# Kernel tuning notes

Hardware: AMD Instinct MI355X
Metric: run time of the kernel (lower is better)

## Reference

```python
import jax, jax.numpy as jnp
import numpy as np

B, NV, NK = 256, 10475, 144
MV, MK = 778, 21
NB, KN = 8192, 9
TOT_ITR, SW = 5, 0.5


def axis_angle_to_matrix(aa):
    # Rodrigues formula, aa: [B,3] -> [B,3,3]
    angle = jnp.linalg.norm(aa, axis=-1, keepdims=True)
    axis = aa / (angle + 1e-8)
    x, y, z = axis[..., 0], axis[..., 1], axis[..., 2]
    c = jnp.cos(angle[..., 0]); s = jnp.sin(angle[..., 0]); C = 1.0 - c
    R = jnp.stack([
        jnp.stack([c + x * x * C, x * y * C - z * s, x * z * C + y * s], -1),
        jnp.stack([y * x * C + z * s, c + y * y * C, y * z * C - x * s], -1),
        jnp.stack([z * x * C - y * s, z * y * C + x * s, c + z * z * C], -1)], -2)
    return R


def rigid_align(X, Y):
    # Umeyama w/o scale (pytorch3d corresponding_points_alignment): X @ R + T ~= Y
    muX = X.mean(1, keepdims=True); muY = Y.mean(1, keepdims=True)
    C = jnp.einsum('bni,bnj->bij', X - muX, Y - muY)
    U, S, Vt = jnp.linalg.svd(C)
    d = jnp.sign(jnp.linalg.det(U) * jnp.linalg.det(Vt))
    e = jnp.stack([jnp.ones_like(d), jnp.ones_like(d), d], -1)
    R = jnp.einsum('bij,bj,bjk->bik', U, e, Vt)
    T = muY[:, 0] - jnp.einsum('bi,bij->bj', muX[:, 0], R)
    return R, T


def combine_smplx_mano(smplx_vert, smplx_kpt, rv, rk, rpose, lv, lk, lpose,
                       rigid_align_idx, r_align_smplx, l_align_smplx,
                       rhand_vertex_idx, lhand_vertex_idx, r_kpt_idx, l_kpt_idx):
    # undo hand root rotation (torch.inverse on rotation matrices)
    Rr = jnp.linalg.inv(axis_angle_to_matrix(rpose))
    rv = jnp.einsum('bij,bnj->bni', Rr, rv); rk = jnp.einsum('bij,bnj->bni', Rr, rk)
    Rl = jnp.linalg.inv(axis_angle_to_matrix(lpose))
    lv = jnp.einsum('bij,bnj->bni', Rl, lv); lk = jnp.einsum('bij,bnj->bni', Rl, lk)
    # rigid alignment of MANO keypoints to SMPL-X hand keypoints
    R, T = rigid_align(rk[:, rigid_align_idx], smplx_kpt[:, r_align_smplx])
    rv = jnp.einsum('bni,bij->bnj', rv, R) + T[:, None]
    rk = jnp.einsum('bni,bij->bnj', rk, R) + T[:, None]
    R, T = rigid_align(lk[:, rigid_align_idx], smplx_kpt[:, l_align_smplx])
    lv = jnp.einsum('bni,bij->bnj', lv, R) + T[:, None]
    lk = jnp.einsum('bni,bij->bnj', lk, R) + T[:, None]
    # scatter MANO verts/kpts into SMPL-X mesh (torch scatter_ -> .at[].set)
    smplx_vert = smplx_vert.at[:, rhand_vertex_idx].set(rv)
    smplx_vert = smplx_vert.at[:, lhand_vertex_idx].set(lv)
    smplx_kpt = smplx_kpt.at[:, r_kpt_idx].set(rk)
    smplx_kpt = smplx_kpt.at[:, l_kpt_idx].set(lk)
    return smplx_vert, smplx_kpt


def smooth_hand_boundary(v, hand_boundary_idx, vert_neighbor_idxs):
    vn = vert_neighbor_idxs[hand_boundary_idx]                     # [NB, KN]
    mask = vn != -1
    safe = jnp.where(mask, vn, 0)
    num_valid = jnp.maximum(mask.sum(-1), 1).astype(v.dtype)        # [NB]
    maskf = mask.astype(v.dtype)[None, :, :, None]
    for _ in range(TOT_ITR):
        npos = v[:, safe] * maskf                                   # [B, NB, KN, 3]
        nmean = npos.sum(2) / num_valid[None, :, None]
        upd = (1.0 - SW) * v[:, hand_boundary_idx] + SW * nmean
        v = v.at[:, hand_boundary_idx].set(upd)
    return v


def setup_inputs():
    key = jax.random.key(0)
    k = jax.random.split(key, 8)
    rng = np.random.default_rng(0)
    vperm = rng.permutation(NV)
    kperm = rng.permutation(NK)
    vn = rng.integers(0, NV, size=(NV, KN))
    vn[rng.random((NV, KN)) < 0.2] = -1  # -1 padding like smpl_x.vert_neighbor_idxs
    return {
        'smplx_vert_cam': jax.random.normal(k[0], (B, NV, 3), jnp.float32),
        'smplx_kpt_cam': jax.random.normal(k[1], (B, NK, 3), jnp.float32),
        'rmano_vert_cam': jax.random.normal(k[2], (B, MV, 3), jnp.float32),
        'rmano_kpt_cam': jax.random.normal(k[3], (B, MK, 3), jnp.float32),
        'rhand_root_pose': jax.random.normal(k[4], (B, 3), jnp.float32),
        'lmano_vert_cam': jax.random.normal(k[5], (B, MV, 3), jnp.float32),
        'lmano_kpt_cam': jax.random.normal(k[6], (B, MK, 3), jnp.float32),
        'lhand_root_pose': jax.random.normal(k[7], (B, 3), jnp.float32),
        'rigid_align_idx': jnp.asarray(rng.permutation(MK), jnp.int32),
        'r_align_smplx': jnp.asarray(kperm[:MK], jnp.int32),
        'l_align_smplx': jnp.asarray(kperm[MK:2 * MK], jnp.int32),
        'rhand_vertex_idx': jnp.asarray(vperm[:MV], jnp.int32),
        'lhand_vertex_idx': jnp.asarray(vperm[MV:2 * MV], jnp.int32),
        'r_kpt_idx': jnp.asarray(kperm[:MK], jnp.int32),
        'l_kpt_idx': jnp.asarray(kperm[MK:2 * MK], jnp.int32),
        'hand_boundary_idx': jnp.asarray(rng.choice(NV, NB, replace=False), jnp.int32),
        'vert_neighbor_idxs': jnp.asarray(vn, jnp.int32),
    }


def reference(smplx_vert_cam, smplx_kpt_cam, rmano_vert_cam, rmano_kpt_cam,
              rhand_root_pose, lmano_vert_cam, lmano_kpt_cam, lhand_root_pose,
              rigid_align_idx, r_align_smplx, l_align_smplx,
              rhand_vertex_idx, lhand_vertex_idx, r_kpt_idx, l_kpt_idx,
              hand_boundary_idx, vert_neighbor_idxs):
    v, _ = combine_smplx_mano(
        smplx_vert_cam, smplx_kpt_cam, rmano_vert_cam, rmano_kpt_cam,
        rhand_root_pose, lmano_vert_cam, lmano_kpt_cam, lhand_root_pose,
        rigid_align_idx, r_align_smplx, l_align_smplx,
        rhand_vertex_idx, lhand_vertex_idx, r_kpt_idx, l_kpt_idx)
    v = smooth_hand_boundary(v, hand_boundary_idx, vert_neighbor_idxs)
    return v
```

## Files before the change

### kernel.cpp

```cpp
#include <hip/hip_runtime.h>

#define BB    256
#define NVERT 10475
#define NKPT  144
#define MVERT 778
#define MKPT  21
#define NBDRY 8192
#define KNB   9
#define ITERS 5
#define NV3   (NVERT * 3)
#define MV3   (MVERT * 3)

typedef float f32x4 __attribute__((ext_vector_type(4)));

static __device__ __forceinline__ float bfu(unsigned hi16) {
    return __uint_as_float(hi16);
}
static __device__ __forceinline__ unsigned f2bf(float f) {
    unsigned u = __float_as_uint(f);
    u += 0x7FFFu + ((u >> 16) & 1u);
    return u >> 16;
}

static __device__ __forceinline__ void pack_one(unsigned short* msh16, unsigned p, float val) {
    unsigned v = p / 3u;
    unsigned c = p - v * 3u;
    msh16[v * 4u + c] = (unsigned short)f2bf(val);
}

static __device__ __forceinline__ void stage_load(const float* __restrict__ g,
                                                  float* sh, int n, int t, int nt) {
    unsigned lead = (4u - ((unsigned)(((size_t)g) >> 2) & 3u)) & 3u;
    unsigned nb4 = ((unsigned)n - lead) >> 2;
    if (t == 0) for (unsigned e = 0; e < lead; ++e) sh[e] = g[e];
    if (t == 1) for (unsigned e = lead + 4u * nb4; e < (unsigned)n; ++e) sh[e] = g[e];
    const f32x4* g4 = (const f32x4*)(g + lead);
    for (unsigned i4 = (unsigned)t; i4 < nb4; i4 += (unsigned)nt) {
        f32x4 q = g4[i4];
        unsigned p = lead + 4u * i4;
        sh[p] = q.x; sh[p + 1] = q.y; sh[p + 2] = q.z; sh[p + 3] = q.w;
    }
}

static __device__ void compute_align(
    int b, int h,
    const float* __restrict__ skpt, const float* __restrict__ rkpt,
    const float* __restrict__ lkpt, const float* __restrict__ rpose,
    const float* __restrict__ lpose, const int* __restrict__ perm,
    const int* __restrict__ ralign, const int* __restrict__ lalign,
    float* o)
{
    const float* pose = (h ? lpose : rpose) + b * 3;
    const float* kpt  = (h ? lkpt : rkpt) + (size_t)b * MKPT * 3;
    const int* alidx  = h ? lalign : ralign;

    float ax = pose[0], ay = pose[1], az = pose[2];
    float ang = sqrtf(ax*ax + ay*ay + az*az);
    float ia = 1.0f / (ang + 1e-8f);
    float x = ax*ia, y = ay*ia, z = az*ia;
    float c = cosf(ang), s = sinf(ang), Cc = 1.0f - c;
    float A00 = c + x*x*Cc,   A01 = x*y*Cc - z*s, A02 = x*z*Cc + y*s;
    float A10 = y*x*Cc + z*s, A11 = c + y*y*Cc,   A12 = y*z*Cc - x*s;
    float A20 = z*x*Cc - y*s, A21 = z*y*Cc + x*s, A22 = c + z*z*Cc;

    float sX0=0,sX1=0,sX2=0, sY0=0,sY1=0,sY2=0;
    float S00=0,S01=0,S02=0,S10=0,S11=0,S12=0,S20=0,S21=0,S22=0;
    for (int n = 0; n < MKPT; ++n) {
        int pi = perm[n];
        float p0 = kpt[pi*3+0], p1 = kpt[pi*3+1], p2 = kpt[pi*3+2];
        float X0 = A00*p0 + A10*p1 + A20*p2;
        float X1 = A01*p0 + A11*p1 + A21*p2;
        float X2 = A02*p0 + A12*p1 + A22*p2;
        int qi = alidx[n];
        const float* yp = skpt + ((size_t)b * NKPT + qi) * 3;
        float Y0 = yp[0], Y1 = yp[1], Y2 = yp[2];
        sX0 += X0; sX1 += X1; sX2 += X2;
        sY0 += Y0; sY1 += Y1; sY2 += Y2;
        S00 += X0*Y0; S01 += X0*Y1; S02 += X0*Y2;
        S10 += X1*Y0; S11 += X1*Y1; S12 += X1*Y2;
        S20 += X2*Y0; S21 += X2*Y1; S22 += X2*Y2;
    }
    const float invN = 1.0f / (float)MKPT;
    float C00 = S00 - sX0*sY0*invN, C01 = S01 - sX0*sY1*invN, C02 = S02 - sX0*sY2*invN;
    float C10 = S10 - sX1*sY0*invN, C11 = S11 - sX1*sY1*invN, C12 = S12 - sX1*sY2*invN;
    float C20 = S20 - sX2*sY0*invN, C21 = S21 - sX2*sY1*invN, C22 = S22 - sX2*sY2*invN;

    float N[4][4];
    N[0][0] = C00 + C11 + C22;
    N[0][1] = C21 - C12; N[0][2] = C02 - C20; N[0][3] = C10 - C01;
    N[1][1] = C00 - C11 - C22; N[1][2] = C01 + C10; N[1][3] = C02 + C20;
    N[2][2] = -C00 + C11 - C22; N[2][3] = C12 + C21;
    N[3][3] = -C00 - C11 + C22;
    N[1][0] = N[0][1]; N[2][0] = N[0][2]; N[3][0] = N[0][3];
    N[2][1] = N[1][2]; N[3][1] = N[1][3]; N[3][2] = N[2][3];

    float V[4][4] = {{1,0,0,0},{0,1,0,0},{0,0,1,0},{0,0,0,1}};
    for (int sweep = 0; sweep < 10; ++sweep) {
        float off = N[0][1]*N[0][1] + N[0][2]*N[0][2] + N[0][3]*N[0][3]
                  + N[1][2]*N[1][2] + N[1][3]*N[1][3] + N[2][3]*N[2][3];
        if (off < 1e-12f) break;
        #pragma unroll
        for (int p = 0; p < 3; ++p) {
            #pragma unroll
            for (int q = p + 1; q < 4; ++q) {
                float apq = N[p][q];
                if (fabsf(apq) > 1e-30f) {
                    float theta = (N[q][q] - N[p][p]) / (2.0f * apq);
                    float tt = copysignf(1.0f, theta) / (fabsf(theta) + sqrtf(theta*theta + 1.0f));
                    float cj = rsqrtf(tt*tt + 1.0f);
                    float sj = tt * cj;
                    #pragma unroll
                    for (int k = 0; k < 4; ++k) {
                        float akp = N[k][p], akq = N[k][q];
                        N[k][p] = cj*akp - sj*akq;
                        N[k][q] = sj*akp + cj*akq;
                    }
                    #pragma unroll
                    for (int k = 0; k < 4; ++k) {
                        float apk = N[p][k], aqk = N[q][k];
                        N[p][k] = cj*apk - sj*aqk;
                        N[q][k] = sj*apk + cj*aqk;
                    }
                    #pragma unroll
                    for (int k = 0; k < 4; ++k) {
                        float vkp = V[k][p], vkq = V[k][q];
                        V[k][p] = cj*vkp - sj*vkq;
                        V[k][q] = sj*vkp + cj*vkq;
                    }
                }
            }
        }
    }
    int m = 0;
    float lmax = N[0][0];
    if (N[1][1] > lmax) { lmax = N[1][1]; m = 1; }
    if (N[2][2] > lmax) { lmax = N[2][2]; m = 2; }
    if (N[3][3] > lmax) { lmax = N[3][3]; m = 3; }
    float w = V[0][m], qx = V[1][m], qy = V[2][m], qz = V[3][m];

    float R00 = 1.0f - 2.0f*(qy*qy + qz*qz), R01 = 2.0f*(qx*qy - w*qz), R02 = 2.0f*(qx*qz + w*qy);
    float R10 = 2.0f*(qx*qy + w*qz), R11 = 1.0f - 2.0f*(qx*qx + qz*qz), R12 = 2.0f*(qy*qz - w*qx);
    float R20 = 2.0f*(qx*qz - w*qy), R21 = 2.0f*(qy*qz + w*qx), R22 = 1.0f - 2.0f*(qx*qx + qy*qy);

    float mX0 = sX0*invN, mX1 = sX1*invN, mX2 = sX2*invN;
    float mY0 = sY0*invN, mY1 = sY1*invN, mY2 = sY2*invN;

    o[0]  = A00*R00 + A01*R10 + A02*R20;
    o[1]  = A00*R01 + A01*R11 + A02*R21;
    o[2]  = A00*R02 + A01*R12 + A02*R22;
    o[3]  = A10*R00 + A11*R10 + A12*R20;
    o[4]  = A10*R01 + A11*R11 + A12*R21;
    o[5]  = A10*R02 + A11*R12 + A12*R22;
    o[6]  = A20*R00 + A21*R10 + A22*R20;
    o[7]  = A20*R01 + A21*R11 + A22*R21;
    o[8]  = A20*R02 + A21*R12 + A22*R22;
    o[9]  = mY0 - (mX0*R00 + mX1*R10 + mX2*R20);
    o[10] = mY1 - (mX0*R01 + mX1*R11 + mX2*R21);
    o[11] = mY2 - (mX0*R02 + mX1*R12 + mX2*R22);
}

__global__ __launch_bounds__(1024, 1) void fused_kernel(
    const float* __restrict__ svert,
    const float* __restrict__ skpt,
    const float* __restrict__ rv,
    const float* __restrict__ rkpt,
    const float* __restrict__ rpose,
    const float* __restrict__ lv,
    const float* __restrict__ lkpt,
    const float* __restrict__ lpose,
    const int*   __restrict__ perm,
    const int*   __restrict__ ralign,
    const int*   __restrict__ lalign,
    const int*   __restrict__ ridx,
    const int*   __restrict__ lidx,
    const int*   __restrict__ bidx,
    const int*   __restrict__ vnbr,
    float*       __restrict__ out)
{
    __shared__ __align__(16) unsigned short msh16[(NVERT + 1) * 4];
    __shared__ __align__(16) float hstage[2 * MV3];
    __shared__ float affsh[24];
    const int b = blockIdx.x;
    const int tid = threadIdx.x;

    if (tid < 2) {
        compute_align(b, tid, skpt, rkpt, lkpt, rpose, lpose,
                      perm, ralign, lalign, affsh + tid * 12);
    } else if (tid == 2) {
        *((uint2*)(msh16 + NVERT * 4)) = make_uint2(0u, 0u);
    } else if (tid >= 64) {
        const int t = tid - 64;
        const float* g = svert + (size_t)b * NV3;
        unsigned lead = (4u - ((unsigned)(((size_t)g) >> 2) & 3u)) & 3u;
        unsigned nb4 = ((unsigned)NV3 - lead) >> 2;
        if (t == 0) for (unsigned e = 0; e < lead; ++e) pack_one(msh16, e, g[e]);
        if (t == 1) for (unsigned e = lead + 4u * nb4; e < (unsigned)NV3; ++e) pack_one(msh16, e, g[e]);
        const f32x4* g4 = (const f32x4*)(g + lead);
        for (unsigned i4 = (unsigned)t; i4 < nb4; i4 += 960u) {
            f32x4 q = g4[i4];
            unsigned p = lead + 4u * i4;
            pack_one(msh16, p,     q.x);
            pack_one(msh16, p + 1, q.y);
            pack_one(msh16, p + 2, q.z);
            pack_one(msh16, p + 3, q.w);
        }
        stage_load(rv + (size_t)b * MV3, hstage,       MV3, t, 960);
        stage_load(lv + (size_t)b * MV3, hstage + MV3, MV3, t, 960);
    }

    unsigned w0[8], w1[8], w2[8], w3[8], w4[8];
    #pragma unroll
    for (int k = 0; k < 8; ++k) {
        int j = k * 1024 + tid;
        int bi = bidx[j];
        const int* row = vnbr + (size_t)bi * KNB;
        unsigned n[9]; unsigned cnt = 0;
        #pragma unroll
        for (int e = 0; e < 9; ++e) {
            int vv = row[e];
            if (vv >= 0) { n[e] = (unsigned)vv; ++cnt; }
            else         { n[e] = (unsigned)NVERT; }
        }
        if (cnt == 0) cnt = 1;
        w0[k] = n[0] | (n[1] << 14);
        w1[k] = n[2] | (n[3] << 14);
        w2[k] = n[4] | (n[5] << 14);
        w3[k] = n[6] | (n[7] << 14);
        w4[k] = n[8] | ((unsigned)bi << 14) | (cnt << 28);
    }
    __syncthreads();

    for (int i = tid; i < 2 * MVERT; i += 1024) {
        int h = (i >= MVERT) ? 1 : 0;
        int nn = i - h * MVERT;
        const int* hidx = h ? lidx : ridx;
        const float* M = affsh + h * 12;
        const float* p = hstage + h * MV3 + nn * 3;
        float p0 = p[0], p1 = p[1], p2 = p[2];
        float o0 = p0 * M[0] + p1 * M[3] + p2 * M[6] + M[9];
        float o1 = p0 * M[1] + p1 * M[4] + p2 * M[7] + M[10];
        float o2 = p0 * M[2] + p1 * M[5] + p2 * M[8] + M[11];
        ((uint2*)msh16)[hidx[nn]] = make_uint2(f2bf(o0) | (f2bf(o1) << 16), f2bf(o2));
    }
    __syncthreads();

    const uint2* mesh = (const uint2*)msh16;

#define NB_GATHER(idx) { uint2 m = mesh[(idx)]; \
        sx += bfu(m.x << 16); sy += bfu(m.x & 0xFFFF0000u); sz += bfu(m.y << 16); }
    for (int itr = 0; itr < ITERS; ++itr) {
        uint2 up[8];
        #pragma unroll
        for (int k = 0; k < 8; ++k) {
            float sx = 0.f, sy = 0.f, sz = 0.f;
            NB_GATHER(w0[k] & 0x3FFFu);
            NB_GATHER((w0[k] >> 14) & 0x3FFFu);
            NB_GATHER(w1[k] & 0x3FFFu);
            NB_GATHER((w1[k] >> 14) & 0x3FFFu);
            NB_GATHER(w2[k] & 0x3FFFu);
            NB_GATHER((w2[k] >> 14) & 0x3FFFu);
            NB_GATHER(w3[k] & 0x3FFFu);
            NB_GATHER((w3[k] >> 14) & 0x3FFFu);
            NB_GATHER(w4[k] & 0x3FFFu);
            uint2 ms = mesh[(w4[k] >> 14) & 0x3FFFu];
            float hinv = 0.5f * __builtin_amdgcn_rcpf((float)(w4[k] >> 28));
            float ux = 0.5f * bfu(ms.x << 16)         + hinv * sx;
            float uy = 0.5f * bfu(ms.x & 0xFFFF0000u) + hinv * sy;
            float uz = 0.5f * bfu(ms.y << 16)         + hinv * sz;
            up[k] = make_uint2(f2bf(ux) | (f2bf(uy) << 16), f2bf(uz));
        }
        __syncthreads();
        #pragma unroll
        for (int k = 0; k < 8; ++k) {
            ((uint2*)msh16)[(w4[k] >> 14) & 0x3FFFu] = up[k];
        }
        __syncthreads();
    }
#undef NB_GATHER

    float* dst = out + (size_t)b * NV3;
    const unsigned lead = (4u - ((unsigned)(((size_t)dst) >> 2) & 3u)) & 3u;
#define COMP(i, val) { unsigned v_ = (i) / 3u; unsigned c_ = (i) - v_ * 3u; \
        uint2 m_ = mesh[v_]; \
        val = (c_ == 0u) ? bfu(m_.x << 16) : (c_ == 1u) ? bfu(m_.x & 0xFFFF0000u) : bfu(m_.y << 16); }
    if ((unsigned)tid < lead) {
        float v; COMP((unsigned)tid, v);
        dst[tid] = v;
    }
    const unsigned nb4 = ((unsigned)NV3 - lead) >> 2;
    f32x4* dst4 = (f32x4*)(dst + lead);
    for (unsigned i4 = (unsigned)tid; i4 < nb4; i4 += 1024u) {
        unsigned i0 = lead + 4u * i4;
        f32x4 o;
        COMP(i0 + 0u, o.x);
        COMP(i0 + 1u, o.y);
        COMP(i0 + 2u, o.z);
        COMP(i0 + 3u, o.w);
        dst4[i4] = o;
    }
    const unsigned done = lead + 4u * nb4;
    if ((unsigned)tid < (unsigned)NV3 - done) {
        float v; COMP(done + (unsigned)tid, v);
        dst[done + tid] = v;
    }
#undef COMP
}

extern "C" void kernel_launch(void* const* d_in, const int* in_sizes, int n_in,
                              void* d_out, int out_size, void* d_ws, size_t ws_size,
                              hipStream_t stream) {
    const float* svert  = (const float*)d_in[0];
    const float* skpt   = (const float*)d_in[1];
    const float* rv     = (const float*)d_in[2];
    const float* rk     = (const float*)d_in[3];
    const float* rpose  = (const float*)d_in[4];
    const float* lv     = (const float*)d_in[5];
    const float* lk     = (const float*)d_in[6];
    const float* lpose  = (const float*)d_in[7];
    const int*   perm   = (const int*)d_in[8];
    const int*   ralign = (const int*)d_in[9];
    const int*   lalign = (const int*)d_in[10];
    const int*   ridx   = (const int*)d_in[11];
    const int*   lidx   = (const int*)d_in[12];
    const int*   bidx   = (const int*)d_in[15];
    const int*   vnbr   = (const int*)d_in[16];
    float* out = (float*)d_out;

    fused_kernel<<<BB, 1024, 0, stream>>>(svert, skpt, rv, rk, rpose,
                                          lv, lk, lpose, perm, ralign, lalign,
                                          ridx, lidx, bidx, vnbr, out);
}
```

Before: 68.83 us.

## Precompute alignment and neighbor tables in a setup kernel before the fused smoothing kernel

Adds a small setup kernel that computes the per-batch rigid-alignment affines and the packed boundary-neighbor index table once, writing both to workspace. Previously every block redid the neighbor packing and ran the serial SVD alignment on two threads. The main kernel now reads these precomputed values, so all 1024 threads take part in the mesh load. It also keeps each boundary vertex's own value in registers across iterations, removing one LDS read per update, which is valid because only that thread writes the vertex. The cost is an extra kernel launch and the global round trip of the table.

After: 64.17 us. -6.8%, faster.

```diff
diff --git a/kernel.cpp b/kernel.cpp
--- a/kernel.cpp
+++ b/kernel.cpp
@@ -159,22 +159,47 @@
     o[11] = mY2 - (mX0*R02 + mX1*R12 + mX2*R22);
 }
 
+__global__ __launch_bounds__(128) void setup_kernel(
+    const float* __restrict__ skpt, const float* __restrict__ rkpt,
+    const float* __restrict__ lkpt, const float* __restrict__ rpose,
+    const float* __restrict__ lpose, const int* __restrict__ perm,
+    const int* __restrict__ ralign, const int* __restrict__ lalign,
+    const int* __restrict__ bidx, const int* __restrict__ vnbr,
+    float* __restrict__ aff, unsigned* __restrict__ tab)
+{
+    const int g = blockIdx.x;
+    if (g < 4) {
+        int t = g * 128 + threadIdx.x;
+        compute_align(t >> 1, t & 1, skpt, rkpt, lkpt, rpose, lpose,
+                      perm, ralign, lalign, aff + t * 12);
+        return;
+    }
+    int j = (g - 4) * 128 + threadIdx.x;
+    int bi = bidx[j];
+    const int* row = vnbr + (size_t)bi * KNB;
+    unsigned n[9]; unsigned cnt = 0;
+    #pragma unroll
+    for (int e = 0; e < 9; ++e) {
+        int vv = row[e];
+        if (vv >= 0) { n[e] = (unsigned)vv; ++cnt; }
+        else         { n[e] = (unsigned)NVERT; }
+    }
+    if (cnt == 0) cnt = 1;
+    tab[0 * NBDRY + j] = n[0] | (n[1] << 14);
+    tab[1 * NBDRY + j] = n[2] | (n[3] << 14);
+    tab[2 * NBDRY + j] = n[4] | (n[5] << 14);
+    tab[3 * NBDRY + j] = n[6] | (n[7] << 14);
+    tab[4 * NBDRY + j] = n[8] | ((unsigned)bi << 14) | (cnt << 28);
+}
+
 __global__ __launch_bounds__(1024, 1) void fused_kernel(
     const float* __restrict__ svert,
-    const float* __restrict__ skpt,
     const float* __restrict__ rv,
-    const float* __restrict__ rkpt,
-    const float* __restrict__ rpose,
     const float* __restrict__ lv,
-    const float* __restrict__ lkpt,
-    const float* __restrict__ lpose,
-    const int*   __restrict__ perm,
-    const int*   __restrict__ ralign,
-    const int*   __restrict__ lalign,
     const int*   __restrict__ ridx,
     const int*   __restrict__ lidx,
-    const int*   __restrict__ bidx,
-    const int*   __restrict__ vnbr,
+    const float* __restrict__ aff,
+    const unsigned* __restrict__ tab,
     float*       __restrict__ out)
 {
     __shared__ __align__(16) unsigned short msh16[(NVERT + 1) * 4];
@@ -183,20 +208,16 @@
     const int b = blockIdx.x;
     const int tid = threadIdx.x;
 
-    if (tid < 2) {
-        compute_align(b, tid, skpt, rkpt, lkpt, rpose, lpose,
-                      perm, ralign, lalign, affsh + tid * 12);
-    } else if (tid == 2) {
-        *((uint2*)(msh16 + NVERT * 4)) = make_uint2(0u, 0u);
-    } else if (tid >= 64) {
-        const int t = tid - 64;
+    if (tid == 0) *((uint2*)(msh16 + NVERT * 4)) = make_uint2(0u, 0u);
+    if (tid < 24) affsh[tid] = aff[b * 24 + tid];
+    {
         const float* g = svert + (size_t)b * NV3;
         unsigned lead = (4u - ((unsigned)(((size_t)g) >> 2) & 3u)) & 3u;
         unsigned nb4 = ((unsigned)NV3 - lead) >> 2;
-        if (t == 0) for (unsigned e = 0; e < lead; ++e) pack_one(msh16, e, g[e]);
-        if (t == 1) for (unsigned e = lead + 4u * nb4; e < (unsigned)NV3; ++e) pack_one(msh16, e, g[e]);
+        if (tid == 0) for (unsigned e = 0; e < lead; ++e) pack_one(msh16, e, g[e]);
+        if (tid == 1) for (unsigned e = lead + 4u * nb4; e < (unsigned)NV3; ++e) pack_one(msh16, e, g[e]);
         const f32x4* g4 = (const f32x4*)(g + lead);
-        for (unsigned i4 = (unsigned)t; i4 < nb4; i4 += 960u) {
+        for (unsigned i4 = (unsigned)tid; i4 < nb4; i4 += 1024u) {
             f32x4 q = g4[i4];
             unsigned p = lead + 4u * i4;
             pack_one(msh16, p,     q.x);
@@ -204,29 +225,18 @@
             pack_one(msh16, p + 2, q.z);
             pack_one(msh16, p + 3, q.w);
         }
-        stage_load(rv + (size_t)b * MV3, hstage,       MV3, t, 960);
-        stage_load(lv + (size_t)b * MV3, hstage + MV3, MV3, t, 960);
-    }
-
+        stage_load(rv + (size_t)b * MV3, hstage,       MV3, tid, 1024);
+        stage_load(lv + (size_t)b * MV3, hstage + MV3, MV3, tid, 1024);
+    }
     unsigned w0[8], w1[8], w2[8], w3[8], w4[8];
     #pragma unroll
     for (int k = 0; k < 8; ++k) {
         int j = k * 1024 + tid;
-        int bi = bidx[j];
-        const int* row = vnbr + (size_t)bi * KNB;
-        unsigned n[9]; unsigned cnt = 0;
-        #pragma unroll
-        for (int e = 0; e < 9; ++e) {
-            int vv = row[e];
-            if (vv >= 0) { n[e] = (unsigned)vv; ++cnt; }
-            else         { n[e] = (unsigned)NVERT; }
-        }
-        if (cnt == 0) cnt = 1;
-        w0[k] = n[0] | (n[1] << 14);
-        w1[k] = n[2] | (n[3] << 14);
-        w2[k] = n[4] | (n[5] << 14);
-        w3[k] = n[6] | (n[7] << 14);
-        w4[k] = n[8] | ((unsigned)bi << 14) | (cnt << 28);
+        w0[k] = tab[j];
+        w1[k] = tab[NBDRY + j];
+        w2[k] = tab[2 * NBDRY + j];
+        w3[k] = tab[3 * NBDRY + j];
+        w4[k] = tab[4 * NBDRY + j];
     }
     __syncthreads();
 
@@ -246,10 +256,13 @@
 
     const uint2* mesh = (const uint2*)msh16;
 
+    uint2 up[8];
+    #pragma unroll
+    for (int k = 0; k < 8; ++k) up[k] = mesh[(w4[k] >> 14) & 0x3FFFu];
+
 #define NB_GATHER(idx) { uint2 m = mesh[(idx)]; \
         sx += bfu(m.x << 16); sy += bfu(m.x & 0xFFFF0000u); sz += bfu(m.y << 16); }
     for (int itr = 0; itr < ITERS; ++itr) {
-        uint2 up[8];
         #pragma unroll
         for (int k = 0; k < 8; ++k) {
             float sx = 0.f, sy = 0.f, sz = 0.f;
@@ -262,11 +275,10 @@
             NB_GATHER(w3[k] & 0x3FFFu);
             NB_GATHER((w3[k] >> 14) & 0x3FFFu);
             NB_GATHER(w4[k] & 0x3FFFu);
-            uint2 ms = mesh[(w4[k] >> 14) & 0x3FFFu];
             float hinv = 0.5f * __builtin_amdgcn_rcpf((float)(w4[k] >> 28));
-            float ux = 0.5f * bfu(ms.x << 16)         + hinv * sx;
-            float uy = 0.5f * bfu(ms.x & 0xFFFF0000u) + hinv * sy;
-            float uz = 0.5f * bfu(ms.y << 16)         + hinv * sz;
+            float ux = 0.5f * bfu(up[k].x << 16)         + hinv * sx;
+            float uy = 0.5f * bfu(up[k].x & 0xFFFF0000u) + hinv * sy;
+            float uz = 0.5f * bfu(up[k].y << 16)         + hinv * sz;
             up[k] = make_uint2(f2bf(ux) | (f2bf(uy) << 16), f2bf(uz));
         }
         __syncthreads();
@@ -326,7 +338,12 @@
     const int*   vnbr   = (const int*)d_in[16];
     float* out = (float*)d_out;
 
-    fused_kernel<<<BB, 1024, 0, stream>>>(svert, skpt, rv, rk, rpose,
-                                          lv, lk, lpose, perm, ralign, lalign,
-                                          ridx, lidx, bidx, vnbr, out);
-}
+    float*    aff = (float*)d_ws;
+    unsigned* tab = (unsigned*)((char*)d_ws + 24576);
+
+    setup_kernel<<<68, 128, 0, stream>>>(skpt, rk, lk, rpose, lpose,
+                                         perm, ralign, lalign, bidx, vnbr,
+                                         aff, tab);
+    fused_kernel<<<BB, 1024, 0, stream>>>(svert, rv, lv, ridx, lidx,
+                                          aff, tab, out);
+}
```

## Precompute static neighbor sums once and gather only dynamic boundary neighbors per iteration

Applied to the files above, without the earlier changes.

A new pre-kernel builds a per-boundary-vertex table that splits neighbors into those that belong to the boundary set (and change across iterations) and those that do not (and stay constant). The main kernel sums the static neighbors once into shared memory and re-gathers only the dynamic neighbors in each of the five smoothing iterations, cutting LDS gather traffic. It also vectorizes the bf16 mesh pack and unpack so that whole 12-float groups are handled per thread. The cost is an extra kernel launch, a larger shared-memory pool, and one more bf16 rounding on the static partial sum, which could shift numerics slightly.

Result: slower. 84.96 us (+23.4%).

```diff
diff --git a/kernel.cpp b/kernel.cpp
--- a/kernel.cpp
+++ b/kernel.cpp
@@ -21,7 +21,9 @@
     u += 0x7FFFu + ((u >> 16) & 1u);
     return u >> 16;
 }
-
+static __device__ __forceinline__ uint2 packv(float x, float y, float z) {
+    return make_uint2(f2bf(x) | (f2bf(y) << 16), f2bf(z));
+}
 static __device__ __forceinline__ void pack_one(unsigned short* msh16, unsigned p, float val) {
     unsigned v = p / 3u;
     unsigned c = p - v * 3u;
@@ -159,6 +161,40 @@
     o[11] = mY2 - (mX0*R02 + mX1*R12 + mX2*R22);
 }
 
+__global__ __launch_bounds__(128) void pack_kernel(
+    const int* __restrict__ bidx, const int* __restrict__ vnbr,
+    unsigned* __restrict__ tab)
+{
+    __shared__ unsigned char flag[NVERT];
+    const int tid = threadIdx.x;
+    for (int i = tid; i < NVERT; i += 128) flag[i] = 0;
+    __syncthreads();
+    for (int j = tid; j < NBDRY; j += 128) flag[bidx[j]] = 1;
+    __syncthreads();
+    int j = blockIdx.x * 128 + tid;
+    int bi = bidx[j];
+    const int* row = vnbr + (size_t)bi * KNB;
+    unsigned slot[9];
+    #pragma unroll
+    for (int e = 0; e < 9; ++e) slot[e] = (unsigned)NVERT;
+    int dc = 0, sc = 0;
+    #pragma unroll
+    for (int e = 0; e < 9; ++e) {
+        int v = row[e];
+        if (v >= 0) {
+            if (flag[v]) slot[dc++] = (unsigned)v;
+            else         slot[8 - (sc++)] = (unsigned)v;
+        }
+    }
+    unsigned vcnt = (unsigned)(dc + sc);
+    if (vcnt == 0u) vcnt = 1u;
+    tab[0 * NBDRY + j] = slot[0] | (slot[1] << 14) | ((unsigned)dc << 28);
+    tab[1 * NBDRY + j] = slot[2] | (slot[3] << 14) | (vcnt << 28);
+    tab[2 * NBDRY + j] = slot[4] | (slot[5] << 14);
+    tab[3 * NBDRY + j] = slot[6] | (slot[7] << 14);
+    tab[4 * NBDRY + j] = slot[8] | ((unsigned)bi << 14) | ((unsigned)sc << 28);
+}
+
 __global__ __launch_bounds__(1024, 1) void fused_kernel(
     const float* __restrict__ svert,
     const float* __restrict__ skpt,
@@ -173,13 +209,15 @@
     const int*   __restrict__ lalign,
     const int*   __restrict__ ridx,
     const int*   __restrict__ lidx,
-    const int*   __restrict__ bidx,
-    const int*   __restrict__ vnbr,
+    const unsigned* __restrict__ tab,
     float*       __restrict__ out)
 {
-    __shared__ __align__(16) unsigned short msh16[(NVERT + 1) * 4];
-    __shared__ __align__(16) float hstage[2 * MV3];
+    __shared__ __align__(16) unsigned long long pool64[(83808 + 65536) / 8];
     __shared__ float affsh[24];
+    unsigned short* msh16 = (unsigned short*)pool64;
+    uint2* meshw = (uint2*)pool64;
+    float* hstage = (float*)((char*)pool64 + 83808);
+    uint2* ssum   = (uint2*)((char*)pool64 + 83808);
     const int b = blockIdx.x;
     const int tid = threadIdx.x;
 
@@ -187,22 +225,47 @@
         compute_align(b, tid, skpt, rkpt, lkpt, rpose, lpose,
                       perm, ralign, lalign, affsh + tid * 12);
     } else if (tid == 2) {
-        *((uint2*)(msh16 + NVERT * 4)) = make_uint2(0u, 0u);
+        meshw[NVERT] = make_uint2(0u, 0u);
     } else if (tid >= 64) {
         const int t = tid - 64;
         const float* g = svert + (size_t)b * NV3;
         unsigned lead = (4u - ((unsigned)(((size_t)g) >> 2) & 3u)) & 3u;
-        unsigned nb4 = ((unsigned)NV3 - lead) >> 2;
-        if (t == 0) for (unsigned e = 0; e < lead; ++e) pack_one(msh16, e, g[e]);
-        if (t == 1) for (unsigned e = lead + 4u * nb4; e < (unsigned)NV3; ++e) pack_one(msh16, e, g[e]);
-        const f32x4* g4 = (const f32x4*)(g + lead);
-        for (unsigned i4 = (unsigned)t; i4 < nb4; i4 += 960u) {
-            f32x4 q = g4[i4];
-            unsigned p = lead + 4u * i4;
-            pack_one(msh16, p,     q.x);
-            pack_one(msh16, p + 1, q.y);
-            pack_one(msh16, p + 2, q.z);
-            pack_one(msh16, p + 3, q.w);
+        unsigned r0 = lead % 3u;
+        unsigned qb = (lead - r0) / 3u;
+        unsigned ng = ((unsigned)NV3 - lead) / 12u;
+        const f32x4* s4 = (const f32x4*)(g + lead);
+        if (t == 0) for (unsigned d = 0; d < lead; ++d) pack_one(msh16, d, g[d]);
+        if (t == 1) for (unsigned d = lead + 12u * ng; d < (unsigned)NV3; ++d) pack_one(msh16, d, g[d]);
+        if (r0 == 0u) {
+            for (unsigned gi = (unsigned)t; gi < ng; gi += 960u) {
+                f32x4 a = s4[3*gi], c = s4[3*gi+1], e = s4[3*gi+2];
+                unsigned q = qb + 4u * gi;
+                meshw[q]     = packv(a.x, a.y, a.z);
+                meshw[q + 1] = packv(a.w, c.x, c.y);
+                meshw[q + 2] = packv(c.z, c.w, e.x);
+                meshw[q + 3] = packv(e.y, e.z, e.w);
+            }
+        } else if (r0 == 1u) {
+            for (unsigned gi = (unsigned)t; gi < ng; gi += 960u) {
+                f32x4 a = s4[3*gi], c = s4[3*gi+1], e = s4[3*gi+2];
+                unsigned q = qb + 4u * gi;
+                msh16[4u*q + 1] = (unsigned short)f2bf(a.x);
+                msh16[4u*q + 2] = (unsigned short)f2bf(a.y);
+                meshw[q + 1] = packv(a.z, a.w, c.x);
+                meshw[q + 2] = packv(c.y, c.z, c.w);
+                meshw[q + 3] = packv(e.x, e.y, e.z);
+                msh16[4u*(q + 4)] = (unsigned short)f2bf(e.w);
+            }
+        } else {
+            for (unsigned gi = (unsigned)t; gi < ng; gi += 960u) {
+                f32x4 a = s4[3*gi], c = s4[3*gi+1], e = s4[3*gi+2];
+                unsigned q = qb + 4u * gi;
+                msh16[4u*q + 2] = (unsigned short)f2bf(a.x);
+                meshw[q + 1] = packv(a.y, a.z, a.w);
+                meshw[q + 2] = packv(c.x, c.y, c.z);
+                meshw[q + 3] = packv(c.w, e.x, e.y);
+                ((unsigned*)msh16)[2u*(q + 4)] = f2bf(e.z) | (f2bf(e.w) << 16);
+            }
         }
         stage_load(rv + (size_t)b * MV3, hstage,       MV3, t, 960);
         stage_load(lv + (size_t)b * MV3, hstage + MV3, MV3, t, 960);
@@ -212,21 +275,11 @@
     #pragma unroll
     for (int k = 0; k < 8; ++k) {
         int j = k * 1024 + tid;
-        int bi = bidx[j];
-        const int* row = vnbr + (size_t)bi * KNB;
-        unsigned n[9]; unsigned cnt = 0;
-        #pragma unroll
-        for (int e = 0; e < 9; ++e) {
-            int vv = row[e];
-            if (vv >= 0) { n[e] = (unsigned)vv; ++cnt; }
-            else         { n[e] = (unsigned)NVERT; }
-        }
-        if (cnt == 0) cnt = 1;
-        w0[k] = n[0] | (n[1] << 14);
-        w1[k] = n[2] | (n[3] << 14);
-        w2[k] = n[4] | (n[5] << 14);
-        w3[k] = n[6] | (n[7] << 14);
-        w4[k] = n[8] | ((unsigned)bi << 14) | (cnt << 28);
+        w0[k] = tab[j];
+        w1[k] = tab[NBDRY + j];
+        w2[k] = tab[2 * NBDRY + j];
+        w3[k] = tab[3 * NBDRY + j];
+        w4[k] = tab[4 * NBDRY + j];
     }
     __syncthreads();
 
@@ -240,70 +293,106 @@
         float o0 = p0 * M[0] + p1 * M[3] + p2 * M[6] + M[9];
         float o1 = p0 * M[1] + p1 * M[4] + p2 * M[7] + M[10];
         float o2 = p0 * M[2] + p1 * M[5] + p2 * M[8] + M[11];
-        ((uint2*)msh16)[hidx[nn]] = make_uint2(f2bf(o0) | (f2bf(o1) << 16), f2bf(o2));
+        meshw[hidx[nn]] = packv(o0, o1, o2);
     }
     __syncthreads();
 
-    const uint2* mesh = (const uint2*)msh16;
-
-#define NB_GATHER(idx) { uint2 m = mesh[(idx)]; \
-        sx += bfu(m.x << 16); sy += bfu(m.x & 0xFFFF0000u); sz += bfu(m.y << 16); }
+#define ADD3(IDX, X, Y, Z) { uint2 m_ = meshw[(IDX)]; \
+        X += bfu(m_.x << 16); Y += bfu(m_.x & 0xFFFF0000u); Z += bfu(m_.y << 16); }
+
+    uint2 up[8];
+    #pragma unroll
+    for (int k = 0; k < 8; ++k) {
+        unsigned a0 = w0[k], a1 = w1[k], a2 = w2[k], a3 = w3[k], a4 = w4[k];
+        up[k] = meshw[(a4 >> 14) & 0x3FFFu];
+        int sc = (int)(a4 >> 28);
+        float tx = 0.f, ty = 0.f, tz = 0.f;
+        if (sc > 0) ADD3(a4 & 0x3FFFu, tx, ty, tz)
+        if (sc > 1) ADD3((a3 >> 14) & 0x3FFFu, tx, ty, tz)
+        if (sc > 2) ADD3(a3 & 0x3FFFu, tx, ty, tz)
+        if (sc > 3) ADD3((a2 >> 14) & 0x3FFFu, tx, ty, tz)
+        if (sc > 4) ADD3(a2 & 0x3FFFu, tx, ty, tz)
+        if (sc > 5) ADD3((a1 >> 14) & 0x3FFFu, tx, ty, tz)
+        if (sc > 6) ADD3(a1 & 0x3FFFu, tx, ty, tz)
+        if (sc > 7) ADD3((a0 >> 14) & 0x3FFFu, tx, ty, tz)
+        if (sc > 8) ADD3(a0 & 0x3FFFu, tx, ty, tz)
+        ssum[k * 1024 + tid] = packv(tx, ty, tz);
+    }
+
     for (int itr = 0; itr < ITERS; ++itr) {
-        uint2 up[8];
         #pragma unroll
         for (int k = 0; k < 8; ++k) {
-            float sx = 0.f, sy = 0.f, sz = 0.f;
-            NB_GATHER(w0[k] & 0x3FFFu);
-            NB_GATHER((w0[k] >> 14) & 0x3FFFu);
-            NB_GATHER(w1[k] & 0x3FFFu);
-            NB_GATHER((w1[k] >> 14) & 0x3FFFu);
-            NB_GATHER(w2[k] & 0x3FFFu);
-            NB_GATHER((w2[k] >> 14) & 0x3FFFu);
-            NB_GATHER(w3[k] & 0x3FFFu);
-            NB_GATHER((w3[k] >> 14) & 0x3FFFu);
-            NB_GATHER(w4[k] & 0x3FFFu);
-            uint2 ms = mesh[(w4[k] >> 14) & 0x3FFFu];
-            float hinv = 0.5f * __builtin_amdgcn_rcpf((float)(w4[k] >> 28));
-            float ux = 0.5f * bfu(ms.x << 16)         + hinv * sx;
-            float uy = 0.5f * bfu(ms.x & 0xFFFF0000u) + hinv * sy;
-            float uz = 0.5f * bfu(ms.y << 16)         + hinv * sz;
-            up[k] = make_uint2(f2bf(ux) | (f2bf(uy) << 16), f2bf(uz));
+            unsigned a0 = w0[k], a1 = w1[k], a2 = w2[k], a3 = w3[k], a4 = w4[k];
+            int dc = (int)(a0 >> 28);
+            uint2 sv = ssum[k * 1024 + tid];
+            float sx = bfu(sv.x << 16), sy = bfu(sv.x & 0xFFFF0000u), sz = bfu(sv.y << 16);
+            if (dc > 0) ADD3(a0 & 0x3FFFu, sx, sy, sz)
+            if (dc > 1) ADD3((a0 >> 14) & 0x3FFFu, sx, sy, sz)
+            if (dc > 2) ADD3(a1 & 0x3FFFu, sx, sy, sz)
+            if (dc > 3) ADD3((a1 >> 14) & 0x3FFFu, sx, sy, sz)
+            if (dc > 4) ADD3(a2 & 0x3FFFu, sx, sy, sz)
+            if (dc > 5) ADD3((a2 >> 14) & 0x3FFFu, sx, sy, sz)
+            if (dc > 6) ADD3(a3 & 0x3FFFu, sx, sy, sz)
+            if (dc > 7) ADD3((a3 >> 14) & 0x3FFFu, sx, sy, sz)
+            if (dc > 8) ADD3(a4 & 0x3FFFu, sx, sy, sz)
+            float hinv = 0.5f * __builtin_amdgcn_rcpf((float)(a1 >> 28));
+            float ux = 0.5f * bfu(up[k].x << 16)         + hinv * sx;
+            float uy = 0.5f * bfu(up[k].x & 0xFFFF0000u) + hinv * sy;
+            float uz = 0.5f * bfu(up[k].y << 16)         + hinv * sz;
+            up[k] = packv(ux, uy, uz);
         }
         __syncthreads();
         #pragma unroll
         for (int k = 0; k < 8; ++k) {
-            ((uint2*)msh16)[(w4[k] >> 14) & 0x3FFFu] = up[k];
+            meshw[(w4[k] >> 14) & 0x3FFFu] = up[k];
         }
         __syncthreads();
     }
-#undef NB_GATHER
+#undef ADD3
 
     float* dst = out + (size_t)b * NV3;
     const unsigned lead = (4u - ((unsigned)(((size_t)dst) >> 2) & 3u)) & 3u;
+    const unsigned r0 = lead % 3u;
+    const unsigned qb = (lead - r0) / 3u;
+    const unsigned ng = ((unsigned)NV3 - lead) / 12u;
+    f32x4* d4 = (f32x4*)(dst + lead);
 #define COMP(i, val) { unsigned v_ = (i) / 3u; unsigned c_ = (i) - v_ * 3u; \
-        uint2 m_ = mesh[v_]; \
+        uint2 m_ = meshw[v_]; \
         val = (c_ == 0u) ? bfu(m_.x << 16) : (c_ == 1u) ? bfu(m_.x & 0xFFFF0000u) : bfu(m_.y << 16); }
-    if ((unsigned)tid < lead) {
-        float v; COMP((unsigned)tid, v);
-        dst[tid] = v;
-    }
-    const unsigned nb4 = ((unsigned)NV3 - lead) >> 2;
-    f32x4* dst4 = (f32x4*)(dst + lead);
-    for (unsigned i4 = (unsigned)tid; i4 < nb4; i4 += 1024u) {
-        unsigned i0 = lead + 4u * i4;
-        f32x4 o;
-        COMP(i0 + 0u, o.x);
-        COMP(i0 + 1u, o.y);
-        COMP(i0 + 2u, o.z);
-        COMP(i0 + 3u, o.w);
-        dst4[i4] = o;
-    }
-    const unsigned done = lead + 4u * nb4;
-    if ((unsigned)tid < (unsigned)NV3 - done) {
-        float v; COMP(done + (unsigned)tid, v);
-        dst[done + tid] = v;
+#define MX(m) bfu((m).x << 16)
+#define MY(m) bfu((m).x & 0xFFFF0000u)
+#define MZ(m) bfu((m).y << 16)
+    if (tid == 0) for (unsigned d = 0; d < lead; ++d) { float v; COMP(d, v); dst[d] = v; }
+    if (tid == 1) for (unsigned d = lead + 12u * ng; d < (unsigned)NV3; ++d) { float v; COMP(d, v); dst[d] = v; }
+    if (r0 == 0u) {
+        for (unsigned gi = (unsigned)tid; gi < ng; gi += 1024u) {
+            unsigned q = qb + 4u * gi;
+            uint2 m0 = meshw[q], m1 = meshw[q+1], m2 = meshw[q+2], m3 = meshw[q+3];
+            d4[3*gi]   = (f32x4){MX(m0), MY(m0), MZ(m0), MX(m1)};
+            d4[3*gi+1] = (f32x4){MY(m1), MZ(m1), MX(m2), MY(m2)};
+            d4[3*gi+2] = (f32x4){MZ(m2), MX(m3), MY(m3), MZ(m3)};
+        }
+    } else if (r0 == 1u) {
+        for (unsigned gi = (unsigned)tid; gi < ng; gi += 1024u) {
+            unsigned q = qb + 4u * gi;
+            uint2 m0 = meshw[q], m1 = meshw[q+1], m2 = meshw[q+2], m3 = meshw[q+3], m4 = meshw[q+4];
+            d4[3*gi]   = (f32x4){MY(m0), MZ(m0), MX(m1), MY(m1)};
+            d4[3*gi+1] = (f32x4){MZ(m1), MX(m2), MY(m2), MZ(m2)};
+            d4[3*gi+2] = (f32x4){MX(m3), MY(m3), MZ(m3), MX(m4)};
+        }
+    } else {
+        for (unsigned gi = (unsigned)tid; gi < ng; gi += 1024u) {
+            unsigned q = qb + 4u * gi;
+            uint2 m0 = meshw[q], m1 = meshw[q+1], m2 = meshw[q+2], m3 = meshw[q+3], m4 = meshw[q+4];
+            d4[3*gi]   = (f32x4){MZ(m0), MX(m1), MY(m1), MZ(m1)};
+            d4[3*gi+1] = (f32x4){MX(m2), MY(m2), MZ(m2), MX(m3)};
+            d4[3*gi+2] = (f32x4){MY(m3), MZ(m3), MX(m4), MY(m4)};
+        }
     }
 #undef COMP
+#undef MX
+#undef MY
+#undef MZ
 }
 
 extern "C" void kernel_launch(void* const* d_in, const int* in_sizes, int n_in,
@@ -326,7 +415,10 @@
     const int*   vnbr   = (const int*)d_in[16];
     float* out = (float*)d_out;
 
+    unsigned* tab = (unsigned*)d_ws;
+
+    pack_kernel<<<64, 128, 0, stream>>>(bidx, vnbr, tab);
     fused_kernel<<<BB, 1024, 0, stream>>>(svert, skpt, rv, rk, rpose,
                                           lv, lk, lpose, perm, ralign, lalign,
-                                          ridx, lidx, bidx, vnbr, out);
-}
+                                          ridx, lidx, tab, out);
+}
```

## Precompute packed neighbor table in a separate kernel and carry self value in registers

Applied to the files above, without the earlier changes.

Adds a small pack_kernel that builds the packed 14-bit neighbor-index words for all boundary vertices once into workspace. The main kernel then reads five coalesced words per boundary vertex instead of having every one of the 256 blocks re-read the indirect neighbor rows and redo the packing. It also keeps each boundary vertex's own value in a register across smoothing iterations, which removes one shared-memory load per vertex per iteration. The cost is an extra kernel launch and a workspace dependency.

After: 62.68 us. -8.9%, faster.

```diff
diff --git a/kernel.cpp b/kernel.cpp
--- a/kernel.cpp
+++ b/kernel.cpp
@@ -21,7 +21,6 @@
     u += 0x7FFFu + ((u >> 16) & 1u);
     return u >> 16;
 }
-
 static __device__ __forceinline__ void pack_one(unsigned short* msh16, unsigned p, float val) {
     unsigned v = p / 3u;
     unsigned c = p - v * 3u;
@@ -159,6 +158,28 @@
     o[11] = mY2 - (mX0*R02 + mX1*R12 + mX2*R22);
 }
 
+__global__ __launch_bounds__(128) void pack_kernel(
+    const int* __restrict__ bidx, const int* __restrict__ vnbr,
+    unsigned* __restrict__ tab)
+{
+    int j = blockIdx.x * 128 + threadIdx.x;
+    int bi = bidx[j];
+    const int* row = vnbr + (size_t)bi * KNB;
+    unsigned n[9]; unsigned cnt = 0;
+    #pragma unroll
+    for (int e = 0; e < 9; ++e) {
+        int vv = row[e];
+        if (vv >= 0) { n[e] = (unsigned)vv; ++cnt; }
+        else         { n[e] = (unsigned)NVERT; }
+    }
+    if (cnt == 0) cnt = 1;
+    tab[0 * NBDRY + j] = n[0] | (n[1] << 14);
+    tab[1 * NBDRY + j] = n[2] | (n[3] << 14);
+    tab[2 * NBDRY + j] = n[4] | (n[5] << 14);
+    tab[3 * NBDRY + j] = n[6] | (n[7] << 14);
+    tab[4 * NBDRY + j] = n[8] | ((unsigned)bi << 14) | (cnt << 28);
+}
+
 __global__ __launch_bounds__(1024, 1) void fused_kernel(
     const float* __restrict__ svert,
     const float* __restrict__ skpt,
@@ -173,8 +194,7 @@
     const int*   __restrict__ lalign,
     const int*   __restrict__ ridx,
     const int*   __restrict__ lidx,
-    const int*   __restrict__ bidx,
-    const int*   __restrict__ vnbr,
+    const unsigned* __restrict__ tab,
     float*       __restrict__ out)
 {
     __shared__ __align__(16) unsigned short msh16[(NVERT + 1) * 4];
@@ -212,21 +232,11 @@
     #pragma unroll
     for (int k = 0; k < 8; ++k) {
         int j = k * 1024 + tid;
-        int bi = bidx[j];
-        const int* row = vnbr + (size_t)bi * KNB;
-        unsigned n[9]; unsigned cnt = 0;
-        #pragma unroll
-        for (int e = 0; e < 9; ++e) {
-            int vv = row[e];
-            if (vv >= 0) { n[e] = (unsigned)vv; ++cnt; }
-            else         { n[e] = (unsigned)NVERT; }
-        }
-        if (cnt == 0) cnt = 1;
-        w0[k] = n[0] | (n[1] << 14);
-        w1[k] = n[2] | (n[3] << 14);
-        w2[k] = n[4] | (n[5] << 14);
-        w3[k] = n[6] | (n[7] << 14);
-        w4[k] = n[8] | ((unsigned)bi << 14) | (cnt << 28);
+        w0[k] = tab[j];
+        w1[k] = tab[NBDRY + j];
+        w2[k] = tab[2 * NBDRY + j];
+        w3[k] = tab[3 * NBDRY + j];
+        w4[k] = tab[4 * NBDRY + j];
     }
     __syncthreads();
 
@@ -246,10 +256,13 @@
 
     const uint2* mesh = (const uint2*)msh16;
 
+    uint2 up[8];
+    #pragma unroll
+    for (int k = 0; k < 8; ++k) up[k] = mesh[(w4[k] >> 14) & 0x3FFFu];
+
 #define NB_GATHER(idx) { uint2 m = mesh[(idx)]; \
         sx += bfu(m.x << 16); sy += bfu(m.x & 0xFFFF0000u); sz += bfu(m.y << 16); }
     for (int itr = 0; itr < ITERS; ++itr) {
-        uint2 up[8];
         #pragma unroll
         for (int k = 0; k < 8; ++k) {
             float sx = 0.f, sy = 0.f, sz = 0.f;
@@ -262,11 +275,10 @@
             NB_GATHER(w3[k] & 0x3FFFu);
             NB_GATHER((w3[k] >> 14) & 0x3FFFu);
             NB_GATHER(w4[k] & 0x3FFFu);
-            uint2 ms = mesh[(w4[k] >> 14) & 0x3FFFu];
             float hinv = 0.5f * __builtin_amdgcn_rcpf((float)(w4[k] >> 28));
-            float ux = 0.5f * bfu(ms.x << 16)         + hinv * sx;
-            float uy = 0.5f * bfu(ms.x & 0xFFFF0000u) + hinv * sy;
-            float uz = 0.5f * bfu(ms.y << 16)         + hinv * sz;
+            float ux = 0.5f * bfu(up[k].x << 16)         + hinv * sx;
+            float uy = 0.5f * bfu(up[k].x & 0xFFFF0000u) + hinv * sy;
+            float uz = 0.5f * bfu(up[k].y << 16)         + hinv * sz;
             up[k] = make_uint2(f2bf(ux) | (f2bf(uy) << 16), f2bf(uz));
         }
         __syncthreads();
@@ -326,7 +338,10 @@
     const int*   vnbr   = (const int*)d_in[16];
     float* out = (float*)d_out;
 
+    unsigned* tab = (unsigned*)d_ws;
+
+    pack_kernel<<<64, 128, 0, stream>>>(bidx, vnbr, tab);
     fused_kernel<<<BB, 1024, 0, stream>>>(svert, skpt, rv, rk, rpose,
                                           lv, lk, lpose, perm, ralign, lalign,
-                                          ridx, lidx, bidx, vnbr, out);
-}
+                                          ridx, lidx, tab, out);
+}
```
